# Kernel tuning notes

Hardware: AMD Instinct MI355X
Metric: run time of the kernel (lower is better)

## Reference

```python
import jax, jax.numpy as jnp
import numpy as np

B, NO, O, H = 8, 512, 1024, 16  # batch, num_obj(=max_len=max_len_k), output_size, heads
DH = O // H
SCALE = 1.0 / (DH ** 0.5)
NEG = -1e9


def setup_inputs() -> dict:
    key = jax.random.key(0)
    ks = jax.random.split(key, 16)
    std = 0.02
    inp = {
        "v": jax.random.normal(ks[0], (B, NO, O), jnp.float32),
        "q": jax.random.normal(ks[1], (B, NO, O), jnp.float32),
        "k": jax.random.normal(ks[2], (B, NO, O), jnp.float32),
        "v_mask": jax.random.randint(ks[3], (B, NO), 0, 2, jnp.int32),
        "q_mask": jax.random.randint(ks[4], (B, NO), 0, 2, jnp.int32),
        "k_mask": jax.random.randint(ks[5], (B, NO), 0, 2, jnp.int32),
        # projection weights (stored as [in, out] so x @ W + b)
        "Wv": jax.random.normal(ks[6], (O, 3 * O), jnp.float32) * std,
        "bv": jnp.zeros((3 * O,), jnp.float32),
        "Wq": jax.random.normal(ks[7], (O, 3 * O), jnp.float32) * std,
        "bq": jnp.zeros((3 * O,), jnp.float32),
        "Wk": jax.random.normal(ks[8], (O, 3 * O), jnp.float32) * std,
        "bk": jnp.zeros((3 * O,), jnp.float32),
        "Wvo": jax.random.normal(ks[9], (O + O, O), jnp.float32) * std,   # v_output: [output+v_size, output]
        "bvo": jnp.zeros((O,), jnp.float32),
        "Wko": jax.random.normal(ks[10], (O + O + O, O), jnp.float32) * std,  # k_output: [output+k_size+v_size, output]
        "bko": jnp.zeros((O,), jnp.float32),
    }
    return inp


def _heads(x):
    # [B, L, O] -> [B, L, H, DH]
    b, l, _ = x.shape
    return x.reshape(b, l, H, DH)


def _attn(qh, kh, vh, mask):
    # qh,kh,vh: [B, L, H, DH]; mask: [B, Lk] (0/1)
    s = jnp.einsum('bnhd,bmhd->bhnm', qh, kh)
    # torch applies masked_fill THEN divides by sqrt(dh): replicate exactly
    s = jnp.where(mask[:, None, None, :] == 0, NEG, s) * SCALE
    a = jax.nn.softmax(s, axis=-1)
    out = jnp.einsum('bhnm,bmhd->bnhd', a, vh)
    return out.reshape(out.shape[0], out.shape[1], O)


def reference(v, q, k, v_mask, q_mask, k_mask, Wv, bv, Wq, bq, Wk, bk, Wvo, bvo, Wko, bko):
    vm = v_mask.astype(v.dtype)[:, :, None]
    qm = q_mask.astype(q.dtype)[:, :, None]
    km = k_mask.astype(k.dtype)[:, :, None]

    v_tr = (jax.nn.relu(v) @ Wv + bv) * vm
    q_tr = (jax.nn.relu(q) @ Wq + bq) * qm
    k_tr = (jax.nn.relu(k) @ Wk + bk) * km

    v_k, v_q, v_v = jnp.split(v_tr, 3, axis=2)
    q_k, q_q, q_v = jnp.split(q_tr, 3, axis=2)
    k_k, k_q, k_v = jnp.split(k_tr, 3, axis=2)

    # faithful to source bug: kv_set is split from k_q (values for k2v are k_q)
    vq_update = _attn(_heads(v_q), _heads(q_k), _heads(q_v), q_mask)  # q->v
    vk_update = _attn(_heads(k_q), _heads(k_k), _heads(k_q), k_mask)  # k self, values = k_q

    updated_v = jnp.concatenate([v, vq_update], axis=2) @ Wvo + bvo
    updated_V = jnp.concatenate([v, vq_update, vk_update], axis=2) @ Wko + bko
    return updated_V, updated_v
```

## Files before the change

kernel.cpp:

```cpp
#include <hip/hip_runtime.h>


typedef float  f32x4  __attribute__((ext_vector_type(4)));
typedef short  bf16x8 __attribute__((ext_vector_type(8)));
typedef unsigned short u16;
typedef unsigned short u16x8v __attribute__((ext_vector_type(8)));

constexpr float ATT_SCALE = 0.125f;
constexpr float NEGS      = -1.25e8f;

#define MiB (size_t(1) << 20)
constexpr size_t O_VR_H = 0*MiB,  O_VR_L = 8*MiB;
constexpr size_t O_QR_H = 16*MiB, O_QR_L = 24*MiB;
constexpr size_t O_KR_H = 32*MiB, O_KR_L = 40*MiB;
constexpr size_t O_WP   = 48*MiB;
constexpr size_t O_PO   = 68*MiB;
constexpr size_t O_VT0  = 0*MiB,  O_VT1 = 8*MiB;
constexpr size_t O_OVQ_H= 16*MiB, O_OVQ_L= 24*MiB;
constexpr size_t O_OVK_H= 32*MiB, O_OVK_L= 40*MiB;
constexpr size_t O_V2_H = 48*MiB, O_V2_L = 56*MiB;
constexpr size_t O_WVO_H= 64*MiB, O_WVO_L= 68*MiB;
constexpr size_t O_WKO_H= 72*MiB, O_WKO_L= 78*MiB;

__device__ __forceinline__ u16 f2bf_rne(float x) {
  unsigned u = __float_as_uint(x);
  return (u16)((u + 0x7FFFu + ((u >> 16) & 1u)) >> 16);
}
__device__ __forceinline__ float bf2f(u16 h) {
  return __uint_as_float(((unsigned)h) << 16);
}
__device__ __forceinline__ void gload16(const void* g, void* l) {
  __builtin_amdgcn_global_load_lds(
      (const __attribute__((address_space(1))) unsigned int*)g,
      (__attribute__((address_space(3))) unsigned int*)l, 16, 0, 0);
}
template <int NWG>
__device__ __forceinline__ int xcd_swz(int bid) {
  return (bid & 7) * (NWG >> 3) + (bid >> 3);
}

__global__ __launch_bounds__(256) void prep_act(
    const float* __restrict__ s0, const float* __restrict__ s1, const float* __restrict__ s2,
    char* __restrict__ ws, const int relu,
    const size_t o0h, const size_t o0l, const size_t o1h, const size_t o1l,
    const size_t o2h, const size_t o2l)
{
  const int z = blockIdx.z;
  const float* src = (z == 0) ? s0 : (z == 1) ? s1 : s2;
  u16* dh = (u16*)(ws + ((z == 0) ? o0h : (z == 1) ? o1h : o2h));
  u16* dl = (u16*)(ws + ((z == 0) ? o0l : (z == 1) ? o1l : o2l));
  const int idx = blockIdx.x * 256 + threadIdx.x;
  const int r = idx & 127, kg = (idx >> 7) & 3, kt = (idx >> 9) & 31, rt = idx >> 14;
  const float* p = src + (size_t)(rt * 128 + r) * 1024 + kt * 32 + kg * 8;
  const float4 x0 = ((const float4*)p)[0];
  const float4 x1 = ((const float4*)p)[1];
  const float xv[8] = {x0.x, x0.y, x0.z, x0.w, x1.x, x1.y, x1.z, x1.w};
  u16x8v hv, lv;
#pragma unroll
  for (int e = 0; e < 8; ++e) {
    const float x = relu ? fmaxf(xv[e], 0.f) : xv[e];
    const u16 hi = f2bf_rne(x);
    hv[e] = hi;
    lv[e] = f2bf_rne(x - bf2f(hi));
  }
  *(u16x8v*)(dh + (size_t)idx * 8) = hv;
  *(u16x8v*)(dl + (size_t)idx * 8) = lv;
}

__global__ __launch_bounds__(256) void prep_w(
    const float* __restrict__ W0, const float* __restrict__ W1, const float* __restrict__ W2,
    char* __restrict__ ws, const int mode)
{
  __shared__ float T[32][129];
  const int kt = blockIdx.x, ntile = blockIdx.y, z = blockIdx.z;
  const float* src; int ld, c0, nkt; u16 *dh, *dl;
  if (mode == 0) {
    const int c0s[5] = {1024, 0, 2048, 0, 1024};
    src = (z == 0) ? W0 : (z <= 2) ? W1 : W2;
    ld = 3072; c0 = c0s[z]; nkt = 32;
    dh = (u16*)(ws + O_WP + (size_t)z * 4 * MiB);
    dl = (u16*)(ws + O_WP + (size_t)z * 4 * MiB + 2 * MiB);
  } else if (mode == 1) {
    src = W0; ld = 1024; c0 = 0; nkt = 64;
    dh = (u16*)(ws + O_WVO_H); dl = (u16*)(ws + O_WVO_L);
  } else {
    src = W0; ld = 1024; c0 = 0; nkt = 96;
    dh = (u16*)(ws + O_WKO_H); dl = (u16*)(ws + O_WKO_L);
  }
  const int tid = threadIdx.x;
#pragma unroll
  for (int j = 0; j < 4; ++j) {
    const int p = tid + j * 256;
    const int row = p >> 5, c4 = p & 31;
    const float4 v = *(const float4*)(src + (size_t)(kt * 32 + row) * ld + c0 + ntile * 128 + c4 * 4);
    T[row][c4 * 4 + 0] = v.x; T[row][c4 * 4 + 1] = v.y;
    T[row][c4 * 4 + 2] = v.z; T[row][c4 * 4 + 3] = v.w;
  }
  __syncthreads();
#pragma unroll
  for (int j = 0; j < 2; ++j) {
    const int c = tid + j * 256;
    const int kg = c >> 7, rr = c & 127;
    u16x8v hv, lv;
#pragma unroll
    for (int e = 0; e < 8; ++e) {
      const float x = T[kg * 8 + e][rr];
      const u16 hi = f2bf_rne(x);
      hv[e] = hi;
      lv[e] = f2bf_rne(x - bf2f(hi));
    }
    const size_t off = (size_t)(ntile * nkt + kt) * 4096 + (size_t)c * 8;
    *(u16x8v*)(dh + off) = hv;
    *(u16x8v*)(dl + off) = lv;
  }
}

template <int NM>
__device__ __forceinline__ void sgemm_core(
    const u16* __restrict__ a0h, const u16* __restrict__ a0l,
    const u16* __restrict__ a1h, const u16* __restrict__ a1l,
    const u16* __restrict__ a2h, const u16* __restrict__ a2l,
    const u16* __restrict__ bh,  const u16* __restrict__ bl,
    const int nkt, const int mt, const int nt, f32x4 acc[4][4])
{
  __shared__ __align__(16) u16 lds[4][4096];
  const int tid = threadIdx.x;
  const int wid = tid >> 6, lane = tid & 63;
  const int lr = lane & 15, lg = lane >> 4;
  const int wm = (wid >> 1) * 64, wn = (wid & 1) * 64;
  u16* myl = &lds[wid][0];

  for (int kt = 0; kt < nkt; ++kt) {
    __syncthreads();
    const int p = kt >> 5, kk = kt & 31;
    const u16* ah = (p == 0) ? a0h : (p == 1) ? a1h : a2h;
    const u16* al = (p == 0) ? a0l : (p == 1) ? a1l : a2l;
    const u16* src = nullptr;
    if      (wid == 0) src = ah + (size_t)(mt * 32 + kk) * 4096;
    else if (wid == 1) src = al + (size_t)(mt * 32 + kk) * 4096;
    else if (wid == 2) src = bh + (size_t)(nt * nkt + kt) * 4096;
    else if (NM == 3)  src = bl + (size_t)(nt * nkt + kt) * 4096;
    if (src) {
      const u16* s = src + lane * 8;
#pragma unroll
      for (int i = 0; i < 8; ++i)
        gload16(s + i * 512, myl + i * 512);
    }
    __syncthreads();

    bf16x8 afh[4], afl[4], bfh[4], bfl[4];
#pragma unroll
    for (int i = 0; i < 4; ++i) {
      const int ra = wm + i * 16 + lr;
      const int rb = wn + i * 16 + lr;
      afh[i] = *(const bf16x8*)&lds[0][(lg * 128 + ra) * 8];
      afl[i] = *(const bf16x8*)&lds[1][(lg * 128 + ra) * 8];
      bfh[i] = *(const bf16x8*)&lds[2][(lg * 128 + rb) * 8];
      if (NM == 3) bfl[i] = *(const bf16x8*)&lds[3][(lg * 128 + rb) * 8];
    }
#pragma unroll
    for (int i = 0; i < 4; ++i)
#pragma unroll
      for (int j = 0; j < 4; ++j) {
        acc[i][j] = __builtin_amdgcn_mfma_f32_16x16x32_bf16(afh[i], bfh[j], acc[i][j], 0, 0, 0);
        if (NM == 3)
          acc[i][j] = __builtin_amdgcn_mfma_f32_16x16x32_bf16(afh[i], bfl[j], acc[i][j], 0, 0, 0);
        acc[i][j] = __builtin_amdgcn_mfma_f32_16x16x32_bf16(afl[i], bfh[j], acc[i][j], 0, 0, 0);
      }
  }
}

__global__ __launch_bounds__(256) void proj_gemm(
    char* __restrict__ ws,
    const float* __restrict__ bv, const float* __restrict__ bq, const float* __restrict__ bk,
    const int* __restrict__ vm, const int* __restrict__ qm, const int* __restrict__ km)
{
  const int swz = xcd_swz<1280>(blockIdx.x);
  const int nt = swz & 7, t = swz >> 3;
  const int mt = t & 31, z = t >> 5;

  const u16* ah = (const u16*)(ws + ((z == 0) ? O_VR_H : (z <= 2) ? O_QR_H : O_KR_H));
  const u16* al = (const u16*)(ws + ((z == 0) ? O_VR_L : (z <= 2) ? O_QR_L : O_KR_L));
  const u16* bh = (const u16*)(ws + O_WP + (size_t)z * 4 * MiB);
  const float* bias = (z == 0) ? bv + 1024 : (z == 1) ? bq : (z == 2) ? bq + 2048
                    : (z == 3) ? bk : bk + 1024;
  const int* msk = (z == 0) ? vm : (z <= 2) ? qm : km;
  u16* out = (u16*)(ws + O_PO + (size_t)z * 8 * MiB);

  f32x4 acc[4][4];
#pragma unroll
  for (int i = 0; i < 4; ++i)
#pragma unroll
    for (int j = 0; j < 4; ++j) {
      f32x4 zer = {0.f, 0.f, 0.f, 0.f};
      acc[i][j] = zer;
    }
  sgemm_core<2>(ah, al, ah, al, ah, al, bh, nullptr, 32, mt, nt, acc);

  const int tid = threadIdx.x, wid = tid >> 6, lane = tid & 63;
  const int lr = lane & 15, lg = lane >> 4;
  const int row0 = mt * 128 + (wid >> 1) * 64;
  const int col0 = nt * 128 + (wid & 1) * 64;
#pragma unroll
  for (int i = 0; i < 4; ++i)
#pragma unroll
    for (int r = 0; r < 4; ++r) {
      const int row = row0 + i * 16 + lg * 4 + r;
      const float mf = (float)msk[row];
#pragma unroll
      for (int j = 0; j < 4; ++j) {
        const int col = col0 + j * 16 + lr;
        out[(size_t)row * 1024 + col] = f2bf_rne((acc[i][j][r] + bias[col]) * mf);
      }
    }
}

__global__ __launch_bounds__(256) void transpose_vt(char* __restrict__ ws) {
  const int z = blockIdx.z, bh = blockIdx.y, kb = blockIdx.x;
  const u16* src = (const u16*)(ws + O_PO + (size_t)((z == 0) ? 2 : 4) * 8 * MiB);
  u16* dst = (u16*)(ws + ((z == 0) ? O_VT0 : O_VT1));
  __shared__ __align__(16) u16 T[64][80];
  const int tid = threadIdx.x;
  const int b = bh >> 4, h = bh & 15;
#pragma unroll
  for (int j = 0; j < 2; ++j) {
    const int p = tid + j * 256;
    const int row = p >> 3, sl = p & 7;
    const u16x8v val = *(const u16x8v*)(src + (size_t)(b * 512 + kb * 64 + row) * 1024 + h * 64 + sl * 8);
    *(u16x8v*)&T[row][sl * 8] = val;
  }
  __syncthreads();
#pragma unroll
  for (int j = 0; j < 2; ++j) {
    const int p = tid + j * 256;
    const int d = p >> 3, ks = p & 7;
    u16x8v val;
#pragma unroll
    for (int e = 0; e < 8; ++e) val[e] = T[ks * 8 + e][d];
    *(u16x8v*)(dst + (size_t)(bh * 64 + d) * 512 + kb * 64 + ks * 8) = val;
  }
}

__global__ __launch_bounds__(256) void attn_kernel(
    char* __restrict__ ws, const int* __restrict__ qm, const int* __restrict__ km)
{
  __shared__ __align__(16) u16 Qs[4096], Ks[4096], Vs[4096];
  __shared__ __align__(16) float Ps[4][16 * 68];
  __shared__ int msk[64];
  const int swz = xcd_swz<2048>(blockIdx.x);
  const int qt = swz & 7, h = (swz >> 3) & 15, zz = swz >> 7;
  const int b = zz >> 1, att = zz & 1;
  const int q0 = qt * 64;
  const u16 *Qg, *Kg, *VTg; const int* mg; u16 *Ohp, *Olp;
  if (att == 0) {
    Qg  = (const u16*)(ws + O_PO + 0 * 8 * MiB);
    Kg  = (const u16*)(ws + O_PO + 1 * 8 * MiB);
    VTg = (const u16*)(ws + O_VT0);
    mg = qm; Ohp = (u16*)(ws + O_OVQ_H); Olp = (u16*)(ws + O_OVQ_L);
  } else {
    Qg  = (const u16*)(ws + O_PO + 4 * 8 * MiB);
    Kg  = (const u16*)(ws + O_PO + 3 * 8 * MiB);
    VTg = (const u16*)(ws + O_VT1);
    mg = km; Ohp = (u16*)(ws + O_OVK_H); Olp = (u16*)(ws + O_OVK_L);
  }
  const int tid = threadIdx.x, wid = tid >> 6, lane = tid & 63;
  const int lr = lane & 15, lg = lane >> 4;

#pragma unroll
  for (int i = 0; i < 2; ++i) {
    const int p = wid * 128 + i * 64 + lane;
    const int row = p >> 3, sl = p & 7;
    const u16* src = Qg + (size_t)(b * 512 + q0 + row) * 1024 + h * 64 + ((sl ^ (row & 7)) * 8);
    gload16(src, &Qs[(wid * 128 + i * 64) * 8]);
  }
  __syncthreads();
  const int qrow = wid * 16 + lr;
  const bf16x8 qa0 = *(const bf16x8*)&Qs[(qrow * 8 + ((0 + lg) ^ (qrow & 7))) * 8];
  const bf16x8 qa1 = *(const bf16x8*)&Qs[(qrow * 8 + ((4 + lg) ^ (qrow & 7))) * 8];

  f32x4 oacc[4];
  float mreg[4], lreg[4];
#pragma unroll
  for (int i = 0; i < 4; ++i) {
    f32x4 zer = {0.f, 0.f, 0.f, 0.f};
    oacc[i] = zer; mreg[i] = -3.0e38f; lreg[i] = 0.f;
  }

  for (int kt = 0; kt < 8; ++kt) {
    __syncthreads();
#pragma unroll
    for (int i = 0; i < 2; ++i) {
      const int p = wid * 128 + i * 64 + lane;
      const int row = p >> 3, sl = p & 7;
      const u16* ksrc = Kg + (size_t)(b * 512 + kt * 64 + row) * 1024 + h * 64 + ((sl ^ (row & 7)) * 8);
      gload16(ksrc, &Ks[(wid * 128 + i * 64) * 8]);
      const u16* vsrc = VTg + (size_t)((b * 16 + h) * 64 + row) * 512 + kt * 64 + ((sl ^ (row & 7)) * 8);
      gload16(vsrc, &Vs[(wid * 128 + i * 64) * 8]);
    }
    if (tid < 64) msk[tid] = mg[b * 512 + kt * 64 + tid];
    __syncthreads();

    f32x4 s[4];
#pragma unroll
    for (int nt = 0; nt < 4; ++nt) {
      f32x4 zer = {0.f, 0.f, 0.f, 0.f};
      s[nt] = zer;
      const int kr = nt * 16 + lr;
      const bf16x8 kb0 = *(const bf16x8*)&Ks[(kr * 8 + ((0 + lg) ^ (kr & 7))) * 8];
      const bf16x8 kb1 = *(const bf16x8*)&Ks[(kr * 8 + ((4 + lg) ^ (kr & 7))) * 8];
      s[nt] = __builtin_amdgcn_mfma_f32_16x16x32_bf16(qa0, kb0, s[nt], 0, 0, 0);
      s[nt] = __builtin_amdgcn_mfma_f32_16x16x32_bf16(qa1, kb1, s[nt], 0, 0, 0);
    }
#pragma unroll
    for (int nt = 0; nt < 4; ++nt) {
      const int mk = msk[nt * 16 + lr];
#pragma unroll
      for (int r = 0; r < 4; ++r)
        s[nt][r] = mk ? s[nt][r] * ATT_SCALE : NEGS;
    }
#pragma unroll
    for (int r = 0; r < 4; ++r) {
      float mx = fmaxf(fmaxf(s[0][r], s[1][r]), fmaxf(s[2][r], s[3][r]));
      mx = fmaxf(mx, __shfl_xor(mx, 1)); mx = fmaxf(mx, __shfl_xor(mx, 2));
      mx = fmaxf(mx, __shfl_xor(mx, 4)); mx = fmaxf(mx, __shfl_xor(mx, 8));
      const float nm = fmaxf(mreg[r], mx);
      const float corr = __expf(mreg[r] - nm);
      float ps = 0.f;
#pragma unroll
      for (int nt = 0; nt < 4; ++nt) {
        const float pv = __expf(s[nt][r] - nm);
        s[nt][r] = pv; ps += pv;
      }
      ps += __shfl_xor(ps, 1); ps += __shfl_xor(ps, 2);
      ps += __shfl_xor(ps, 4); ps += __shfl_xor(ps, 8);
      lreg[r] = lreg[r] * corr + ps;
      mreg[r] = nm;
#pragma unroll
      for (int d = 0; d < 4; ++d) oacc[d][r] *= corr;
    }
    float* Pw = &Ps[wid][0];
#pragma unroll
    for (int nt = 0; nt < 4; ++nt)
#pragma unroll
      for (int r = 0; r < 4; ++r)
        Pw[(lg * 4 + r) * 68 + nt * 16 + lr] = s[nt][r];
#pragma unroll
    for (int ks = 0; ks < 2; ++ks) {
      const float* pp = &Pw[lr * 68 + ks * 32 + lg * 8];
      const f32x4 p0 = *(const f32x4*)pp;
      const f32x4 p1 = *(const f32x4*)(pp + 4);
      bf16x8 pa;
      pa[0] = (short)f2bf_rne(p0[0]); pa[1] = (short)f2bf_rne(p0[1]);
      pa[2] = (short)f2bf_rne(p0[2]); pa[3] = (short)f2bf_rne(p0[3]);
      pa[4] = (short)f2bf_rne(p1[0]); pa[5] = (short)f2bf_rne(p1[1]);
      pa[6] = (short)f2bf_rne(p1[2]); pa[7] = (short)f2bf_rne(p1[3]);
#pragma unroll
      for (int d = 0; d < 4; ++d) {
        const int vr = d * 16 + lr;
        const bf16x8 vb = *(const bf16x8*)&Vs[(vr * 8 + ((ks * 4 + lg) ^ (vr & 7))) * 8];
        oacc[d] = __builtin_amdgcn_mfma_f32_16x16x32_bf16(pa, vb, oacc[d], 0, 0, 0);
      }
    }
  }

#pragma unroll
  for (int r = 0; r < 4; ++r) {
    const float inv = 1.0f / lreg[r];
    const int row = b * 512 + q0 + wid * 16 + lg * 4 + r;
    const int rt = row >> 7, rr = row & 127;
#pragma unroll
    for (int d = 0; d < 4; ++d) {
      const int col = h * 64 + d * 16 + lr;
      const int ktc = col >> 5, kg = (col >> 3) & 3, e = col & 7;
      const size_t off = ((((size_t)rt * 32 + ktc) * 4 + kg) * 128 + rr) * 8 + e;
      const float x = oacc[d][r] * inv;
      const u16 hi = f2bf_rne(x);
      Ohp[off] = hi;
      Olp[off] = f2bf_rne(x - bf2f(hi));
    }
  }
}

__global__ __launch_bounds__(256) void out_gemm(
    char* __restrict__ ws, const float* __restrict__ bvo, const float* __restrict__ bko,
    float* __restrict__ dout)
{
  const int swz = xcd_swz<512>(blockIdx.x);
  const int nt = swz & 7, z = (swz >> 3) & 1, mt = swz >> 4;

  const u16* a0h = (const u16*)(ws + O_V2_H);
  const u16* a0l = (const u16*)(ws + O_V2_L);
  const u16* a1h = (const u16*)(ws + O_OVQ_H);
  const u16* a1l = (const u16*)(ws + O_OVQ_L);
  const u16* a2h = (const u16*)(ws + O_OVK_H);
  const u16* a2l = (const u16*)(ws + O_OVK_L);
  const int nkt = z ? 96 : 64;
  const u16* bh = (const u16*)(ws + (z ? O_WKO_H : O_WVO_H));
  const u16* bl = (const u16*)(ws + (z ? O_WKO_L : O_WVO_L));
  const float* bias = z ? bko : bvo;
  float* dst = z ? dout : (dout + (size_t)4096 * 1024);

  f32x4 acc[4][4];
#pragma unroll
  for (int i = 0; i < 4; ++i)
#pragma unroll
    for (int j = 0; j < 4; ++j) {
      f32x4 zer = {0.f, 0.f, 0.f, 0.f};
      acc[i][j] = zer;
    }
  sgemm_core<3>(a0h, a0l, a1h, a1l, a2h, a2l, bh, bl, nkt, mt, nt, acc);

  const int tid = threadIdx.x, wid = tid >> 6, lane = tid & 63;
  const int lr = lane & 15, lg = lane >> 4;
  const int row0 = mt * 128 + (wid >> 1) * 64;
  const int col0 = nt * 128 + (wid & 1) * 64;
#pragma unroll
  for (int i = 0; i < 4; ++i)
#pragma unroll
    for (int r = 0; r < 4; ++r) {
      const int row = row0 + i * 16 + lg * 4 + r;
#pragma unroll
      for (int j = 0; j < 4; ++j) {
        const int col = col0 + j * 16 + lr;
        dst[(size_t)row * 1024 + col] = acc[i][j][r] + bias[col];
      }
    }
}

extern "C" void kernel_launch(void* const* d_in, const int* in_sizes, int n_in,
                              void* d_out, int out_size, void* d_ws, size_t ws_size,
                              hipStream_t stream) {
  const float* v  = (const float*)d_in[0];
  const float* q  = (const float*)d_in[1];
  const float* k  = (const float*)d_in[2];
  const int* vm   = (const int*)d_in[3];
  const int* qm   = (const int*)d_in[4];
  const int* km   = (const int*)d_in[5];
  const float* Wv = (const float*)d_in[6];
  const float* bv = (const float*)d_in[7];
  const float* Wq = (const float*)d_in[8];
  const float* bq = (const float*)d_in[9];
  const float* Wk = (const float*)d_in[10];
  const float* bk = (const float*)d_in[11];
  const float* Wvo = (const float*)d_in[12];
  const float* bvo = (const float*)d_in[13];
  const float* Wko = (const float*)d_in[14];
  const float* bko = (const float*)d_in[15];
  char* ws = (char*)d_ws;
  float* out = (float*)d_out;

  prep_act<<<dim3(2048, 1, 3), 256, 0, stream>>>(v, q, k, ws, 1,
      O_VR_H, O_VR_L, O_QR_H, O_QR_L, O_KR_H, O_KR_L);
  prep_w<<<dim3(32, 8, 5), 256, 0, stream>>>(Wv, Wq, Wk, ws, 0);
  proj_gemm<<<dim3(1280), 256, 0, stream>>>(ws, bv, bq, bk, vm, qm, km);
  transpose_vt<<<dim3(8, 128, 2), 256, 0, stream>>>(ws);
  attn_kernel<<<dim3(2048), 256, 0, stream>>>(ws, qm, km);
  prep_act<<<dim3(2048, 1, 1), 256, 0, stream>>>(v, v, v, ws, 0,
      O_V2_H, O_V2_L, O_V2_H, O_V2_L, O_V2_H, O_V2_L);
  prep_w<<<dim3(64, 8, 1), 256, 0, stream>>>(Wvo, Wvo, Wvo, ws, 1);
  prep_w<<<dim3(96, 8, 1), 256, 0, stream>>>(Wko, Wko, Wko, ws, 2);
  out_gemm<<<dim3(512), 256, 0, stream>>>(ws, bvo, bko, out);
}
```

Before: 462.1 us.

## Double-buffer LDS tiles in split-bf16 GEMM core to overlap loads with MFMA

```diff
diff --git a/kernel.cpp b/kernel.cpp
--- a/kernel.cpp
+++ b/kernel.cpp
@@ -123,15 +123,14 @@
     const u16* __restrict__ bh,  const u16* __restrict__ bl,
     const int nkt, const int mt, const int nt, f32x4 acc[4][4])
 {
-  __shared__ __align__(16) u16 lds[4][4096];
+  constexpr int NB = (NM == 3) ? 4 : 3;
+  __shared__ __align__(16) u16 lds[2][NB][4096];
   const int tid = threadIdx.x;
   const int wid = tid >> 6, lane = tid & 63;
   const int lr = lane & 15, lg = lane >> 4;
   const int wm = (wid >> 1) * 64, wn = (wid & 1) * 64;
-  u16* myl = &lds[wid][0];
-
-  for (int kt = 0; kt < nkt; ++kt) {
-    __syncthreads();
+
+  auto issue = [&](int kt, int buf) {
     const int p = kt >> 5, kk = kt & 31;
     const u16* ah = (p == 0) ? a0h : (p == 1) ? a1h : a2h;
     const u16* al = (p == 0) ? a0l : (p == 1) ? a1l : a2l;
@@ -140,23 +139,36 @@
     else if (wid == 1) src = al + (size_t)(mt * 32 + kk) * 4096;
     else if (wid == 2) src = bh + (size_t)(nt * nkt + kt) * 4096;
     else if (NM == 3)  src = bl + (size_t)(nt * nkt + kt) * 4096;
-    if (src) {
+    if (wid < NB) {
       const u16* s = src + lane * 8;
+      u16* d = &lds[buf][wid][lane * 8];
 #pragma unroll
       for (int i = 0; i < 8; ++i)
-        gload16(s + i * 512, myl + i * 512);
-    }
-    __syncthreads();
+        gload16(s + i * 512, d + i * 512);
+    }
+  };
+
+  issue(0, 0);
+  for (int kt = 0; kt < nkt; ++kt) {
+    const int cur = kt & 1;
+    if (kt + 1 < nkt) {
+      issue(kt + 1, cur ^ 1);
+      asm volatile("s_waitcnt vmcnt(8)" ::: "memory");
+    } else {
+      asm volatile("s_waitcnt vmcnt(0)" ::: "memory");
+    }
+    __builtin_amdgcn_s_barrier();
+    __builtin_amdgcn_sched_barrier(0);
 
     bf16x8 afh[4], afl[4], bfh[4], bfl[4];
 #pragma unroll
     for (int i = 0; i < 4; ++i) {
       const int ra = wm + i * 16 + lr;
       const int rb = wn + i * 16 + lr;
-      afh[i] = *(const bf16x8*)&lds[0][(lg * 128 + ra) * 8];
-      afl[i] = *(const bf16x8*)&lds[1][(lg * 128 + ra) * 8];
-      bfh[i] = *(const bf16x8*)&lds[2][(lg * 128 + rb) * 8];
-      if (NM == 3) bfl[i] = *(const bf16x8*)&lds[3][(lg * 128 + rb) * 8];
+      afh[i] = *(const bf16x8*)&lds[cur][0][(lg * 128 + ra) * 8];
+      afl[i] = *(const bf16x8*)&lds[cur][1][(lg * 128 + ra) * 8];
+      bfh[i] = *(const bf16x8*)&lds[cur][2][(lg * 128 + rb) * 8];
+      if (NM == 3) bfl[i] = *(const bf16x8*)&lds[cur][3][(lg * 128 + rb) * 8];
     }
 #pragma unroll
     for (int i = 0; i < 4; ++i)
@@ -167,6 +179,8 @@
           acc[i][j] = __builtin_amdgcn_mfma_f32_16x16x32_bf16(afh[i], bfl[j], acc[i][j], 0, 0, 0);
         acc[i][j] = __builtin_amdgcn_mfma_f32_16x16x32_bf16(afl[i], bfh[j], acc[i][j], 0, 0, 0);
       }
+    asm volatile("s_waitcnt lgkmcnt(0)" ::: "memory");
+    __builtin_amdgcn_s_barrier();
   }
 }
 
```

Result: no change. 466.9 us (+1.0%).
